# Kernel optimization log

Measured on AMD Instinct MI355X. Metric: run time of the kernel, lower is better.

## Reference

```python
import jax, jax.numpy as jnp
import numpy as np


def _quantize(x, weight):
    # x: (B, D, H, W); weight: (D, K)
    B, D, H, W = x.shape
    K = weight.shape[1]
    xf = x.reshape(B, D, H * W)  # (B, D, N)
    x2 = jnp.sum(xf * xf, axis=1)                      # (B, N)
    cross = jnp.einsum('bdn,dk->bnk', xf, weight)       # (B, N, K)
    e2 = jnp.sum(weight * weight, axis=0)               # (K,)
    d2 = x2[..., None] - 2.0 * cross + e2               # (B, N, K)
    argmin = jnp.argmin(d2, axis=-1)                    # (B, N)
    # gather codes: (B, N, D) -> (B, D, N) -> (B, D, H, W)
    quant = weight.T[argmin]                            # (B, N, D)
    result = jnp.transpose(quant, (0, 2, 1)).reshape(B, D, H, W)
    return result, argmin.reshape(B, H, W)


def setup_inputs() -> dict:
    key = jax.random.key(0)
    k1, k2 = jax.random.split(key)
    x = jax.random.normal(k1, (32, 256, 32, 32), dtype=jnp.float32)
    weight = jax.random.uniform(k2, (256, 512), dtype=jnp.float32)  # torch.rand init
    return {"x": x, "weight": weight}


def reference(x, weight):
    result, argmin = _quantize(x, weight)
    return result, argmin
```

## Files before the change

### kernel.cpp

```cpp
#include <hip/hip_runtime.h>

typedef __attribute__((ext_vector_type(8))) short bf16x8;
typedef __attribute__((ext_vector_type(16))) float f32x16;

__device__ __forceinline__ bool lex_lt(float av, int ai, float bv, int bi) {
  return av < bv || (av == bv && ai < bi);
}

__device__ __forceinline__ unsigned bf16_rne(float v) {
  unsigned u = __float_as_uint(v);
  return (u + 0x7fffu + ((u >> 16) & 1u)) >> 16;
}

__device__ __forceinline__ unsigned pk_bf16(float a, float b) {
  return bf16_rne(a) | (bf16_rne(b) << 16);
}

__global__ __launch_bounds__(256) void vq_pre(
    const float* __restrict__ w, float* __restrict__ e2,
    short* __restrict__ wtil, float* __restrict__ wT) {
  int blk = blockIdx.x;
  if (blk < 64) {
    int gid = blk * 256 + threadIdx.x;
    int n  = gid & 511;
    int kg = gid >> 9;
    bf16x8 hv, lv;
    float vv[8];
#pragma unroll
    for (int j = 0; j < 8; ++j) {
      float v = w[(kg * 8 + j) * 512 + n];
      vv[j] = v;
      unsigned h = bf16_rne(v);
      float hf = __uint_as_float(h << 16);
      unsigned l = bf16_rne(v - hf);
      hv[j] = (short)h;
      lv[j] = (short)l;
    }
    short* dst = wtil + (size_t)gid * 8;
    *(bf16x8*)dst = hv;
    *(bf16x8*)(dst + 131072) = lv;
    if (wT) {
      float* p = wT + (size_t)n * 256 + kg * 8;
      *(float4*)p       = make_float4(vv[0], vv[1], vv[2], vv[3]);
      *(float4*)(p + 4) = make_float4(vv[4], vv[5], vv[6], vv[7]);
    }
  } else {
    int t = (blk - 64) * 256 + threadIdx.x;
    int k = t >> 2;
    int part = t & 3;
    double s = 0.0;
#pragma unroll 8
    for (int d = part * 64; d < part * 64 + 64; ++d) {
      double v = (double)w[d * 512 + k];
      s = fma(v, v, s);
    }
    s += __shfl_xor(s, 1);
    s += __shfl_xor(s, 2);
    if (part == 0) e2[k] = (float)s;
  }
}

__global__ __launch_bounds__(512, 4) void vq_main(
    const float* __restrict__ x, const float* __restrict__ w,
    const float* __restrict__ e2g, const short* __restrict__ wtil,
    const float* __restrict__ wT,
    float* __restrict__ out, float* __restrict__ arg_out) {
  __shared__ __align__(16) char arena[76800];
  short* xh   = (short*)arena;
  short* xl   = (short*)(arena + 32768);
  float* e2s  = (float*)(arena + 65536);
  float* tv1  = (float*)(arena + 67584);
  float* tv2  = (float*)(arena + 69632);
  int*   ti1  = (int*)(arena + 71680);
  int*   ti2  = (int*)(arena + 73728);
  int*   p1S  = (int*)(arena + 75776);
  int*   p2S  = (int*)(arena + 76032);
  int*   needS= (int*)(arena + 76288);
  int*   rpickS=(int*)(arena + 76544);
  float* gbuf = (float*)arena;

  const int tid = threadIdx.x;
  const int b  = blockIdx.x >> 4;
  const int n0 = (blockIdx.x & 15) << 6;
  const float* xbase = x + (size_t)b * 262144 + n0;

  {
    const int n4  = tid & 15;
    const int kgp = tid >> 4;
    float4 v[8];
#pragma unroll
    for (int j = 0; j < 8; ++j)
      v[j] = *(const float4*)(xbase + (size_t)(kgp * 8 + j) * 1024 + (n4 << 2));
#pragma unroll
    for (int i = 0; i < 4; ++i) {
      int m = (n4 << 2) + i;
      union { int w4[4]; bf16x8 v8; } H, L;
#pragma unroll
      for (int jj = 0; jj < 4; ++jj) {
        float a = (i == 0) ? v[2*jj].x : (i == 1) ? v[2*jj].y : (i == 2) ? v[2*jj].z : v[2*jj].w;
        float c = (i == 0) ? v[2*jj+1].x : (i == 1) ? v[2*jj+1].y : (i == 2) ? v[2*jj+1].z : v[2*jj+1].w;
        unsigned hu = pk_bf16(a, c);
        float haf = __uint_as_float(hu << 16);
        float hcf = __uint_as_float(hu & 0xffff0000u);
        unsigned lu = pk_bf16(a - haf, c - hcf);
        H.w4[jj] = (int)hu;
        L.w4[jj] = (int)lu;
      }
      int off = (m << 8) + ((kgp ^ (m & 7)) << 3);
      *(bf16x8*)&xh[off] = H.v8;
      *(bf16x8*)&xl[off] = L.v8;
    }
    e2s[tid] = e2g[tid];
  }
  __syncthreads();

  const int lane = tid & 63;
  const int wv   = tid >> 6;
  const int ln   = lane & 31;
  const int half = lane >> 5;
  const int wb   = wv << 6;

  f32x16 acc[2][2];
#pragma unroll
  for (int ct = 0; ct < 2; ++ct)
#pragma unroll
    for (int pt = 0; pt < 2; ++pt)
#pragma unroll
      for (int r = 0; r < 16; ++r) acc[ct][pt][r] = 0.f;

  const int asw = ln & 7;
  const int abase = ln << 8;

  int bofs[2];
#pragma unroll
  for (int ct = 0; ct < 2; ++ct) bofs[ct] = (wb + (ct << 5) + ln) << 3;

  bf16x8 pch[2], pcl[2];
#pragma unroll
  for (int ct = 0; ct < 2; ++ct) {
    const short* p = wtil + (half << 12) + bofs[ct];
    pch[ct] = *(const bf16x8*)p;
    pcl[ct] = *(const bf16x8*)(p + 131072);
  }

  auto kstep = [&](int ch) {
    const int kg = (ch << 1) + half;
    const int ao = abase + ((kg ^ asw) << 3);
    bf16x8 xf[2], xg[2];
#pragma unroll
    for (int pt = 0; pt < 2; ++pt) {
      xf[pt] = *(const bf16x8*)&xh[ao + (pt << 13)];
      xg[pt] = *(const bf16x8*)&xl[ao + (pt << 13)];
    }
    bf16x8 cfh[2], cfl[2];
#pragma unroll
    for (int ct = 0; ct < 2; ++ct) { cfh[ct] = pch[ct]; cfl[ct] = pcl[ct]; }
    if (ch < 15) {
      const int kgn = ((ch + 1) << 1) + half;
#pragma unroll
      for (int ct = 0; ct < 2; ++ct) {
        const short* p = wtil + (kgn << 12) + bofs[ct];
        pch[ct] = *(const bf16x8*)p;
        pcl[ct] = *(const bf16x8*)(p + 131072);
      }
    }
#pragma unroll
    for (int ct = 0; ct < 2; ++ct)
#pragma unroll
      for (int pt = 0; pt < 2; ++pt) {
        acc[ct][pt] = __builtin_amdgcn_mfma_f32_32x32x16_bf16(cfh[ct], xf[pt], acc[ct][pt], 0, 0, 0);
        acc[ct][pt] = __builtin_amdgcn_mfma_f32_32x32x16_bf16(cfh[ct], xg[pt], acc[ct][pt], 0, 0, 0);
        acc[ct][pt] = __builtin_amdgcn_mfma_f32_32x32x16_bf16(cfl[ct], xf[pt], acc[ct][pt], 0, 0, 0);
      }
  };

  kstep(0);  kstep(1);  kstep(2);  kstep(3);
  kstep(4);  kstep(5);  kstep(6);  kstep(7);
  kstep(8);  kstep(9);  kstep(10); kstep(11);
  kstep(12); kstep(13); kstep(14); kstep(15);

  float e2r[2][16];
#pragma unroll
  for (int ct = 0; ct < 2; ++ct)
#pragma unroll
    for (int r = 0; r < 16; ++r)
      e2r[ct][r] = e2s[wb + (ct << 5) + (r & 3) + ((r >> 2) << 3) + (half << 2)];

#pragma unroll
  for (int pt = 0; pt < 2; ++pt) {
    float v1 = 3.4e38f, v2 = 3.4e38f;
    int i1 = 0x7fffffff, i2 = 0x7fffffff;
#pragma unroll
    for (int ct = 0; ct < 2; ++ct) {
#pragma unroll
      for (int r = 0; r < 16; ++r) {
        int k = wb + (ct << 5) + (r & 3) + ((r >> 2) << 3) + (half << 2);
        float s = fmaf(-2.f, acc[ct][pt][r], e2r[ct][r]);
        if (lex_lt(s, k, v1, i1)) { v2 = v1; i2 = i1; v1 = s; i1 = k; }
        else if (lex_lt(s, k, v2, i2)) { v2 = s; i2 = k; }
      }
    }
    {
      float ov1 = __shfl_xor(v1, 32);
      int   oi1 = __shfl_xor(i1, 32);
      float ov2 = __shfl_xor(v2, 32);
      int   oi2 = __shfl_xor(i2, 32);
      bool aFirst = lex_lt(v1, i1, ov1, oi1);
      float nv1 = aFirst ? v1 : ov1;  int ni1 = aFirst ? i1 : oi1;
      float cv  = aFirst ? ov1 : v1;  int ci  = aFirst ? oi1 : i1;
      float sv  = aFirst ? v2 : ov2;  int si  = aFirst ? i2 : oi2;
      bool cFirst = lex_lt(cv, ci, sv, si);
      v1 = nv1; i1 = ni1;
      v2 = cFirst ? cv : sv; i2 = cFirst ? ci : si;
    }
    if (half == 0) {
      int s = (wv << 6) + (pt << 5) + ln;
      tv1[s] = v1; ti1[s] = i1; tv2[s] = v2; ti2[s] = i2;
    }
  }
  __syncthreads();

  if (tid < 64) {
    int row = tid;
    float v1 = 3.4e38f, v2 = 3.4e38f;
    int i1 = 0x7fffffff, i2 = 0x7fffffff;
#pragma unroll
    for (int wvv = 0; wvv < 8; ++wvv) {
      int s = (wvv << 6) + row;
      float a1 = tv1[s]; int ai = ti1[s];
      float a2 = tv2[s]; int bi = ti2[s];
      if (lex_lt(a1, ai, v1, i1)) { v2 = v1; i2 = i1; v1 = a1; i1 = ai; }
      else if (lex_lt(a1, ai, v2, i2)) { v2 = a1; i2 = ai; }
      if (lex_lt(a2, bi, v1, i1)) { v2 = v1; i2 = i1; v1 = a2; i1 = bi; }
      else if (lex_lt(a2, bi, v2, i2)) { v2 = a2; i2 = bi; }
    }
    p1S[row] = i1; p2S[row] = i2;
    needS[row] = (v2 - v1 < 0.01f) ? 1 : 0;
    rpickS[row] = i1;
  }
  __syncthreads();

  for (int t = 0; t < 8; ++t) {
    int row = (t << 3) + wv;
    if (needS[row]) {
      int i1 = p1S[row], i2 = p2S[row];
      const float* xp = x + (size_t)b * 262144 + n0 + row;
      double s1 = 0.0, s2 = 0.0;
      int k0 = lane << 2;
#pragma unroll
      for (int i = 0; i < 4; ++i) {
        int k = k0 + i;
        double xv = (double)xp[(size_t)k * 1024];
        double w1 = (double)w[k * 512 + i1];
        double w2 = (double)w[k * 512 + i2];
        double t1 = xv - w1, t2 = xv - w2;
        s1 = fma(t1, t1, s1);
        s2 = fma(t2, t2, s2);
      }
#pragma unroll
      for (int off = 32; off >= 1; off >>= 1) {
        s1 += __shfl_xor(s1, off);
        s2 += __shfl_xor(s2, off);
      }
      if (lane == 0 && (s2 < s1 || (s2 == s1 && i2 < i1))) rpickS[row] = i2;
    }
  }
  __syncthreads();

  if (tid < 64) arg_out[b * 1024 + n0 + tid] = (float)rpickS[tid];

  if (wT) {
    {
      const int pos  = tid >> 3;
      const int dseg = tid & 7;
      const float* wrow = wT + (size_t)rpickS[pos] * 256;
#pragma unroll
      for (int j = 0; j < 8; ++j) {
        int d0 = (j << 5) + (dseg << 2);
        float4 v = *(const float4*)(wrow + d0);
        gbuf[(d0 + 0) * 68 + pos] = v.x;
        gbuf[(d0 + 1) * 68 + pos] = v.y;
        gbuf[(d0 + 2) * 68 + pos] = v.z;
        gbuf[(d0 + 3) * 68 + pos] = v.w;
      }
    }
    __syncthreads();
    {
      const int nn0 = (tid & 15) << 2;
      const int d0g = tid >> 4;
      float* obase = out + (size_t)b * 262144 + n0 + nn0;
#pragma unroll
      for (int dg = 0; dg < 8; ++dg) {
        int d = d0g + (dg << 5);
        float4 o = *(const float4*)&gbuf[d * 68 + nn0];
        *(float4*)(obase + (size_t)d * 1024) = o;
      }
    }
  } else {
    const int nn0 = (tid & 15) << 2;
    const int d0g = tid >> 4;
    int pk0 = rpickS[nn0], pk1 = rpickS[nn0 + 1], pk2 = rpickS[nn0 + 2], pk3 = rpickS[nn0 + 3];
    float* obase = out + (size_t)b * 262144 + n0 + nn0;
#pragma unroll
    for (int dg = 0; dg < 8; ++dg) {
      int d = d0g + (dg << 5);
      const float* wr = w + d * 512;
      float4 o = make_float4(wr[pk0], wr[pk1], wr[pk2], wr[pk3]);
      *(float4*)(obase + (size_t)d * 1024) = o;
    }
  }
}

extern "C" void kernel_launch(void* const* d_in, const int* in_sizes, int n_in,
                              void* d_out, int out_size, void* d_ws, size_t ws_size,
                              hipStream_t stream) {
  const float* x = (const float*)d_in[0];
  const float* w = (const float*)d_in[1];
  float* out  = (float*)d_out;
  float* argf = out + 8388608;
  float* e2   = (float*)d_ws;
  short* wtil = (short*)((char*)d_ws + 2048);
  size_t need = 2048 + 524288 + 524288;
  float* wT   = (ws_size >= need) ? (float*)((char*)d_ws + 2048 + 524288) : nullptr;

  vq_pre<<<72, 256, 0, stream>>>(w, e2, wtil, wT);
  vq_main<<<512, 512, 0, stream>>>(x, w, e2, wtil, wT, out, argf);
}
```

Baseline: 115.9 us.

## Fuse codebook preprocessing into main kernel with a software grid barrier

Merges the weight-splitting and codebook-norm kernel into the main VQ kernel. The first 36 blocks do the preprocessing, and all 512 blocks then meet at an atomic grid-wide barrier before the MFMA phase. The goal is to remove a kernel launch and overlap preprocessing with the x conversion into LDS. This relies on all 512 blocks being co-resident: with 4 blocks per CU of 512 threads on 256 CUs that likely holds, but if it does not, the spin-with-timeout break can let blocks read stale data. It also adds a memset launch to reset the barrier counter.

```diff
diff --git a/kernel.cpp b/kernel.cpp
--- a/kernel.cpp
+++ b/kernel.cpp
@@ -16,54 +16,23 @@
   return bf16_rne(a) | (bf16_rne(b) << 16);
 }
 
-__global__ __launch_bounds__(256) void vq_pre(
-    const float* __restrict__ w, float* __restrict__ e2,
-    short* __restrict__ wtil, float* __restrict__ wT) {
-  int blk = blockIdx.x;
-  if (blk < 64) {
-    int gid = blk * 256 + threadIdx.x;
-    int n  = gid & 511;
-    int kg = gid >> 9;
-    bf16x8 hv, lv;
-    float vv[8];
-#pragma unroll
-    for (int j = 0; j < 8; ++j) {
-      float v = w[(kg * 8 + j) * 512 + n];
-      vv[j] = v;
-      unsigned h = bf16_rne(v);
-      float hf = __uint_as_float(h << 16);
-      unsigned l = bf16_rne(v - hf);
-      hv[j] = (short)h;
-      lv[j] = (short)l;
-    }
-    short* dst = wtil + (size_t)gid * 8;
-    *(bf16x8*)dst = hv;
-    *(bf16x8*)(dst + 131072) = lv;
-    if (wT) {
-      float* p = wT + (size_t)n * 256 + kg * 8;
-      *(float4*)p       = make_float4(vv[0], vv[1], vv[2], vv[3]);
-      *(float4*)(p + 4) = make_float4(vv[4], vv[5], vv[6], vv[7]);
-    }
-  } else {
-    int t = (blk - 64) * 256 + threadIdx.x;
-    int k = t >> 2;
-    int part = t & 3;
-    double s = 0.0;
-#pragma unroll 8
-    for (int d = part * 64; d < part * 64 + 64; ++d) {
-      double v = (double)w[d * 512 + k];
-      s = fma(v, v, s);
-    }
-    s += __shfl_xor(s, 1);
-    s += __shfl_xor(s, 2);
-    if (part == 0) e2[k] = (float)s;
-  }
-}
-
-__global__ __launch_bounds__(512, 4) void vq_main(
+__device__ __forceinline__ void grid_barrier(unsigned* bar) {
+  __syncthreads();
+  if (threadIdx.x == 0) {
+    __hip_atomic_fetch_add(bar, 1u, __ATOMIC_RELEASE, __HIP_MEMORY_SCOPE_AGENT);
+    long spins = 0;
+    while (__hip_atomic_load(bar, __ATOMIC_ACQUIRE, __HIP_MEMORY_SCOPE_AGENT) < 512u) {
+      __builtin_amdgcn_s_sleep(1);
+      if (++spins > (1L << 22)) break;
+    }
+  }
+  __syncthreads();
+}
+
+__global__ __launch_bounds__(512, 4) void vq_fused(
     const float* __restrict__ x, const float* __restrict__ w,
-    const float* __restrict__ e2g, const short* __restrict__ wtil,
-    const float* __restrict__ wT,
+    float* __restrict__ e2g, short* __restrict__ wtil,
+    float* __restrict__ wT, unsigned* __restrict__ bar,
     float* __restrict__ out, float* __restrict__ arg_out) {
   __shared__ __align__(16) char arena[76800];
   short* xh   = (short*)arena;
@@ -80,8 +49,49 @@
   float* gbuf = (float*)arena;
 
   const int tid = threadIdx.x;
-  const int b  = blockIdx.x >> 4;
-  const int n0 = (blockIdx.x & 15) << 6;
+  const int bid = blockIdx.x;
+
+  if (bid < 32) {
+    int gid = bid * 512 + tid;
+    int n  = gid & 511;
+    int kg = gid >> 9;
+    bf16x8 hv, lv;
+    float vv[8];
+#pragma unroll
+    for (int j = 0; j < 8; ++j) {
+      float v = w[(kg * 8 + j) * 512 + n];
+      vv[j] = v;
+      unsigned h = bf16_rne(v);
+      float hf = __uint_as_float(h << 16);
+      unsigned l = bf16_rne(v - hf);
+      hv[j] = (short)h;
+      lv[j] = (short)l;
+    }
+    short* dst = wtil + (size_t)gid * 8;
+    *(bf16x8*)dst = hv;
+    *(bf16x8*)(dst + 131072) = lv;
+    if (wT) {
+      float* p = wT + (size_t)n * 256 + kg * 8;
+      *(float4*)p       = make_float4(vv[0], vv[1], vv[2], vv[3]);
+      *(float4*)(p + 4) = make_float4(vv[4], vv[5], vv[6], vv[7]);
+    }
+  } else if (bid < 36) {
+    int t = (bid - 32) * 512 + tid;
+    int k = t >> 2;
+    int part = t & 3;
+    double s = 0.0;
+#pragma unroll 8
+    for (int d = part * 64; d < part * 64 + 64; ++d) {
+      double v = (double)w[d * 512 + k];
+      s = fma(v, v, s);
+    }
+    s += __shfl_xor(s, 1);
+    s += __shfl_xor(s, 2);
+    if (part == 0) e2g[k] = (float)s;
+  }
+
+  const int b  = bid >> 4;
+  const int n0 = (bid & 15) << 6;
   const float* xbase = x + (size_t)b * 262144 + n0;
 
   {
@@ -110,9 +120,9 @@
       *(bf16x8*)&xh[off] = H.v8;
       *(bf16x8*)&xl[off] = L.v8;
     }
-    e2s[tid] = e2g[tid];
-  }
-  __syncthreads();
+  }
+
+  grid_barrier(bar);
 
   const int lane = tid & 63;
   const int wv   = tid >> 6;
@@ -178,6 +188,9 @@
   kstep(4);  kstep(5);  kstep(6);  kstep(7);
   kstep(8);  kstep(9);  kstep(10); kstep(11);
   kstep(12); kstep(13); kstep(14); kstep(15);
+
+  e2s[tid] = e2g[tid];
+  __syncthreads();
 
   float e2r[2][16];
 #pragma unroll
@@ -320,9 +333,10 @@
   float* argf = out + 8388608;
   float* e2   = (float*)d_ws;
   short* wtil = (short*)((char*)d_ws + 2048);
-  size_t need = 2048 + 524288 + 524288;
+  size_t need = 2048 + 524288 + 524288 + (1 << 21) + 64;
   float* wT   = (ws_size >= need) ? (float*)((char*)d_ws + 2048 + 524288) : nullptr;
-
-  vq_pre<<<72, 256, 0, stream>>>(w, e2, wtil, wT);
-  vq_main<<<512, 512, 0, stream>>>(x, w, e2, wtil, wT, out, argf);
-}
+  unsigned* bar = (unsigned*)((char*)d_ws + (1 << 21));
+
+  hipMemsetAsync(bar, 0, 64, stream);
+  vq_fused<<<512, 512, 0, stream>>>(x, w, e2, wtil, wT, bar, out, argf);
+}
```

Measured after the change: 174.7 us. +50.7%, slower.

## Halve per-block position tile to raise occupancy and drop codebook register prefetch

Applied to the files above, without the earlier changes.

Each block now handles 32 positions instead of 64, which halves LDS use and accumulator registers and doubles the grid to 1024 blocks. Launch bounds rise to 8 waves per SIMD. The software prefetch of codebook fragments is replaced by direct loads inside each k-step. Each codebook fragment is now reused by only one position tile instead of two, so global/L2 traffic for the bf16 codebook doubles and load latency is exposed unless the higher occupancy hides it.

```diff
diff --git a/kernel.cpp b/kernel.cpp
--- a/kernel.cpp
+++ b/kernel.cpp
@@ -60,45 +60,46 @@
   }
 }
 
-__global__ __launch_bounds__(512, 4) void vq_main(
+__global__ __launch_bounds__(512, 8) void vq_main(
     const float* __restrict__ x, const float* __restrict__ w,
     const float* __restrict__ e2g, const short* __restrict__ wtil,
     const float* __restrict__ wT,
     float* __restrict__ out, float* __restrict__ arg_out) {
-  __shared__ __align__(16) char arena[76800];
+  __shared__ __align__(16) char arena[39424];
   short* xh   = (short*)arena;
-  short* xl   = (short*)(arena + 32768);
-  float* e2s  = (float*)(arena + 65536);
-  float* tv1  = (float*)(arena + 67584);
-  float* tv2  = (float*)(arena + 69632);
-  int*   ti1  = (int*)(arena + 71680);
-  int*   ti2  = (int*)(arena + 73728);
-  int*   p1S  = (int*)(arena + 75776);
-  int*   p2S  = (int*)(arena + 76032);
-  int*   needS= (int*)(arena + 76288);
-  int*   rpickS=(int*)(arena + 76544);
+  short* xl   = (short*)(arena + 16384);
+  float* e2s  = (float*)(arena + 32768);
+  float* tv1  = (float*)(arena + 34816);
+  float* tv2  = (float*)(arena + 35840);
+  int*   ti1  = (int*)(arena + 36864);
+  int*   ti2  = (int*)(arena + 37888);
+  int*   p1S  = (int*)(arena + 38912);
+  int*   p2S  = (int*)(arena + 39040);
+  int*   needS= (int*)(arena + 39168);
+  int*   rpickS=(int*)(arena + 39296);
   float* gbuf = (float*)arena;
 
   const int tid = threadIdx.x;
-  const int b  = blockIdx.x >> 4;
-  const int n0 = (blockIdx.x & 15) << 6;
+  const int b  = blockIdx.x >> 5;
+  const int n0 = (blockIdx.x & 31) << 5;
   const float* xbase = x + (size_t)b * 262144 + n0;
 
   {
-    const int n4  = tid & 15;
+    e2s[tid] = e2g[tid];
+    const int n2  = tid & 15;
     const int kgp = tid >> 4;
-    float4 v[8];
+    float2 v[8];
 #pragma unroll
     for (int j = 0; j < 8; ++j)
-      v[j] = *(const float4*)(xbase + (size_t)(kgp * 8 + j) * 1024 + (n4 << 2));
-#pragma unroll
-    for (int i = 0; i < 4; ++i) {
-      int m = (n4 << 2) + i;
+      v[j] = *(const float2*)(xbase + (size_t)(kgp * 8 + j) * 1024 + (n2 << 1));
+#pragma unroll
+    for (int i = 0; i < 2; ++i) {
+      int m = (n2 << 1) + i;
       union { int w4[4]; bf16x8 v8; } H, L;
 #pragma unroll
       for (int jj = 0; jj < 4; ++jj) {
-        float a = (i == 0) ? v[2*jj].x : (i == 1) ? v[2*jj].y : (i == 2) ? v[2*jj].z : v[2*jj].w;
-        float c = (i == 0) ? v[2*jj+1].x : (i == 1) ? v[2*jj+1].y : (i == 2) ? v[2*jj+1].z : v[2*jj+1].w;
+        float a = (i == 0) ? v[2*jj].x   : v[2*jj].y;
+        float c = (i == 0) ? v[2*jj+1].x : v[2*jj+1].y;
         unsigned hu = pk_bf16(a, c);
         float haf = __uint_as_float(hu << 16);
         float hcf = __uint_as_float(hu & 0xffff0000u);
@@ -110,7 +111,6 @@
       *(bf16x8*)&xh[off] = H.v8;
       *(bf16x8*)&xl[off] = L.v8;
     }
-    e2s[tid] = e2g[tid];
   }
   __syncthreads();
 
@@ -120,13 +120,11 @@
   const int half = lane >> 5;
   const int wb   = wv << 6;
 
-  f32x16 acc[2][2];
+  f32x16 acc[2];
 #pragma unroll
   for (int ct = 0; ct < 2; ++ct)
 #pragma unroll
-    for (int pt = 0; pt < 2; ++pt)
-#pragma unroll
-      for (int r = 0; r < 16; ++r) acc[ct][pt][r] = 0.f;
+    for (int r = 0; r < 16; ++r) acc[ct][r] = 0.f;
 
   const int asw = ln & 7;
   const int abase = ln << 8;
@@ -134,44 +132,24 @@
   int bofs[2];
 #pragma unroll
   for (int ct = 0; ct < 2; ++ct) bofs[ct] = (wb + (ct << 5) + ln) << 3;
-
-  bf16x8 pch[2], pcl[2];
-#pragma unroll
-  for (int ct = 0; ct < 2; ++ct) {
-    const short* p = wtil + (half << 12) + bofs[ct];
-    pch[ct] = *(const bf16x8*)p;
-    pcl[ct] = *(const bf16x8*)(p + 131072);
-  }
 
   auto kstep = [&](int ch) {
     const int kg = (ch << 1) + half;
     const int ao = abase + ((kg ^ asw) << 3);
-    bf16x8 xf[2], xg[2];
-#pragma unroll
-    for (int pt = 0; pt < 2; ++pt) {
-      xf[pt] = *(const bf16x8*)&xh[ao + (pt << 13)];
-      xg[pt] = *(const bf16x8*)&xl[ao + (pt << 13)];
-    }
-    bf16x8 cfh[2], cfl[2];
-#pragma unroll
-    for (int ct = 0; ct < 2; ++ct) { cfh[ct] = pch[ct]; cfl[ct] = pcl[ct]; }
-    if (ch < 15) {
-      const int kgn = ((ch + 1) << 1) + half;
-#pragma unroll
-      for (int ct = 0; ct < 2; ++ct) {
-        const short* p = wtil + (kgn << 12) + bofs[ct];
-        pch[ct] = *(const bf16x8*)p;
-        pcl[ct] = *(const bf16x8*)(p + 131072);
-      }
-    }
-#pragma unroll
-    for (int ct = 0; ct < 2; ++ct)
-#pragma unroll
-      for (int pt = 0; pt < 2; ++pt) {
-        acc[ct][pt] = __builtin_amdgcn_mfma_f32_32x32x16_bf16(cfh[ct], xf[pt], acc[ct][pt], 0, 0, 0);
-        acc[ct][pt] = __builtin_amdgcn_mfma_f32_32x32x16_bf16(cfh[ct], xg[pt], acc[ct][pt], 0, 0, 0);
-        acc[ct][pt] = __builtin_amdgcn_mfma_f32_32x32x16_bf16(cfl[ct], xf[pt], acc[ct][pt], 0, 0, 0);
-      }
+    bf16x8 xf = *(const bf16x8*)&xh[ao];
+    bf16x8 xg = *(const bf16x8*)&xl[ao];
+    const short* p0 = wtil + (kg << 12) + bofs[0];
+    const short* p1 = wtil + (kg << 12) + bofs[1];
+    bf16x8 ch0 = *(const bf16x8*)p0;
+    bf16x8 cl0 = *(const bf16x8*)(p0 + 131072);
+    bf16x8 ch1 = *(const bf16x8*)p1;
+    bf16x8 cl1 = *(const bf16x8*)(p1 + 131072);
+    acc[0] = __builtin_amdgcn_mfma_f32_32x32x16_bf16(ch0, xf, acc[0], 0, 0, 0);
+    acc[0] = __builtin_amdgcn_mfma_f32_32x32x16_bf16(ch0, xg, acc[0], 0, 0, 0);
+    acc[0] = __builtin_amdgcn_mfma_f32_32x32x16_bf16(cl0, xf, acc[0], 0, 0, 0);
+    acc[1] = __builtin_amdgcn_mfma_f32_32x32x16_bf16(ch1, xf, acc[1], 0, 0, 0);
+    acc[1] = __builtin_amdgcn_mfma_f32_32x32x16_bf16(ch1, xg, acc[1], 0, 0, 0);
+    acc[1] = __builtin_amdgcn_mfma_f32_32x32x16_bf16(cl1, xf, acc[1], 0, 0, 0);
   };
 
   kstep(0);  kstep(1);  kstep(2);  kstep(3);
@@ -179,15 +157,7 @@
   kstep(8);  kstep(9);  kstep(10); kstep(11);
   kstep(12); kstep(13); kstep(14); kstep(15);
 
-  float e2r[2][16];
-#pragma unroll
-  for (int ct = 0; ct < 2; ++ct)
-#pragma unroll
-    for (int r = 0; r < 16; ++r)
-      e2r[ct][r] = e2s[wb + (ct << 5) + (r & 3) + ((r >> 2) << 3) + (half << 2)];
-
-#pragma unroll
-  for (int pt = 0; pt < 2; ++pt) {
+  {
     float v1 = 3.4e38f, v2 = 3.4e38f;
     int i1 = 0x7fffffff, i2 = 0x7fffffff;
 #pragma unroll
@@ -195,7 +165,7 @@
 #pragma unroll
       for (int r = 0; r < 16; ++r) {
         int k = wb + (ct << 5) + (r & 3) + ((r >> 2) << 3) + (half << 2);
-        float s = fmaf(-2.f, acc[ct][pt][r], e2r[ct][r]);
+        float s = fmaf(-2.f, acc[ct][r], e2s[k]);
         if (lex_lt(s, k, v1, i1)) { v2 = v1; i2 = i1; v1 = s; i1 = k; }
         else if (lex_lt(s, k, v2, i2)) { v2 = s; i2 = k; }
       }
@@ -214,19 +184,19 @@
       v2 = cFirst ? cv : sv; i2 = cFirst ? ci : si;
     }
     if (half == 0) {
-      int s = (wv << 6) + (pt << 5) + ln;
+      int s = (wv << 5) + ln;
       tv1[s] = v1; ti1[s] = i1; tv2[s] = v2; ti2[s] = i2;
     }
   }
   __syncthreads();
 
-  if (tid < 64) {
+  if (tid < 32) {
     int row = tid;
     float v1 = 3.4e38f, v2 = 3.4e38f;
     int i1 = 0x7fffffff, i2 = 0x7fffffff;
 #pragma unroll
     for (int wvv = 0; wvv < 8; ++wvv) {
-      int s = (wvv << 6) + row;
+      int s = (wvv << 5) + row;
       float a1 = tv1[s]; int ai = ti1[s];
       float a2 = tv2[s]; int bi = ti2[s];
       if (lex_lt(a1, ai, v1, i1)) { v2 = v1; i2 = i1; v1 = a1; i1 = ai; }
@@ -240,7 +210,7 @@
   }
   __syncthreads();
 
-  for (int t = 0; t < 8; ++t) {
+  for (int t = 0; t < 4; ++t) {
     int row = (t << 3) + wv;
     if (needS[row]) {
       int i1 = p1S[row], i2 = p2S[row];
@@ -267,43 +237,43 @@
   }
   __syncthreads();
 
-  if (tid < 64) arg_out[b * 1024 + n0 + tid] = (float)rpickS[tid];
+  if (tid < 32) arg_out[b * 1024 + n0 + tid] = (float)rpickS[tid];
 
   if (wT) {
     {
-      const int pos  = tid >> 3;
-      const int dseg = tid & 7;
+      const int pos  = tid >> 4;
+      const int dseg = tid & 15;
       const float* wrow = wT + (size_t)rpickS[pos] * 256;
 #pragma unroll
-      for (int j = 0; j < 8; ++j) {
-        int d0 = (j << 5) + (dseg << 2);
+      for (int j = 0; j < 4; ++j) {
+        int d0 = (j << 6) + (dseg << 2);
         float4 v = *(const float4*)(wrow + d0);
-        gbuf[(d0 + 0) * 68 + pos] = v.x;
-        gbuf[(d0 + 1) * 68 + pos] = v.y;
-        gbuf[(d0 + 2) * 68 + pos] = v.z;
-        gbuf[(d0 + 3) * 68 + pos] = v.w;
+        gbuf[(d0 + 0) * 36 + pos] = v.x;
+        gbuf[(d0 + 1) * 36 + pos] = v.y;
+        gbuf[(d0 + 2) * 36 + pos] = v.z;
+        gbuf[(d0 + 3) * 36 + pos] = v.w;
       }
     }
     __syncthreads();
     {
-      const int nn0 = (tid & 15) << 2;
-      const int d0g = tid >> 4;
+      const int nn0 = (tid & 7) << 2;
+      const int d0g = tid >> 3;
       float* obase = out + (size_t)b * 262144 + n0 + nn0;
 #pragma unroll
-      for (int dg = 0; dg < 8; ++dg) {
-        int d = d0g + (dg << 5);
-        float4 o = *(const float4*)&gbuf[d * 68 + nn0];
+      for (int dg = 0; dg < 4; ++dg) {
+        int d = d0g + (dg << 6);
+        float4 o = *(const float4*)&gbuf[d * 36 + nn0];
         *(float4*)(obase + (size_t)d * 1024) = o;
       }
     }
   } else {
-    const int nn0 = (tid & 15) << 2;
-    const int d0g = tid >> 4;
+    const int nn0 = (tid & 7) << 2;
+    const int d0g = tid >> 3;
     int pk0 = rpickS[nn0], pk1 = rpickS[nn0 + 1], pk2 = rpickS[nn0 + 2], pk3 = rpickS[nn0 + 3];
     float* obase = out + (size_t)b * 262144 + n0 + nn0;
 #pragma unroll
-    for (int dg = 0; dg < 8; ++dg) {
-      int d = d0g + (dg << 5);
+    for (int dg = 0; dg < 4; ++dg) {
+      int d = d0g + (dg << 6);
       const float* wr = w + d * 512;
       float4 o = make_float4(wr[pk0], wr[pk1], wr[pk2], wr[pk3]);
       *(float4*)(obase + (size_t)d * 1024) = o;
@@ -324,5 +294,5 @@
   float* wT   = (ws_size >= need) ? (float*)((char*)d_ws + 2048 + 524288) : nullptr;
 
   vq_pre<<<72, 256, 0, stream>>>(w, e2, wtil, wT);
-  vq_main<<<512, 512, 0, stream>>>(x, w, e2, wtil, wT, out, argf);
-}
+  vq_main<<<1024, 512, 0, stream>>>(x, w, e2, wtil, wT, out, argf);
+}
```

Measured after the change: 121.2 us. 1.05x slower.

## Strengthen LDS swizzle, stagger per-wave K start, and prefetch x fragments

Applied to the files above, without the earlier changes.

Adds a second XOR term (row>>3) to the LDS swizzle for the bf16 hi/lo x tiles, intended to remove remaining bank conflicts on the MFMA operand reads. Each wave now starts its K loop at a different chunk offset and wraps around, spreading simultaneous global reads of the codebook across different addresses. The x fragments are also double-buffered in registers alongside the codebook prefetch. Register pressure rises, the loop carries a leftover unused index computation, and accumulation order now differs per wave, which could shift argmin results on near-ties.

```diff
diff --git a/kernel.cpp b/kernel.cpp
--- a/kernel.cpp
+++ b/kernel.cpp
@@ -85,6 +85,7 @@
   const float* xbase = x + (size_t)b * 262144 + n0;
 
   {
+    e2s[tid] = e2g[tid];
     const int n4  = tid & 15;
     const int kgp = tid >> 4;
     float4 v[8];
@@ -106,11 +107,11 @@
         H.w4[jj] = (int)hu;
         L.w4[jj] = (int)lu;
       }
-      int off = (m << 8) + ((kgp ^ (m & 7)) << 3);
+      int slot = kgp ^ (m & 7) ^ ((m >> 3) & 7);
+      int off = (m << 8) + (slot << 3);
       *(bf16x8*)&xh[off] = H.v8;
       *(bf16x8*)&xl[off] = L.v8;
     }
-    e2s[tid] = e2g[tid];
   }
   __syncthreads();
 
@@ -128,56 +129,61 @@
 #pragma unroll
       for (int r = 0; r < 16; ++r) acc[ct][pt][r] = 0.f;
 
-  const int asw = ln & 7;
+  const int sw    = (ln & 7) ^ (ln >> 3);
   const int abase = ln << 8;
 
   int bofs[2];
 #pragma unroll
   for (int ct = 0; ct < 2; ++ct) bofs[ct] = (wb + (ct << 5) + ln) << 3;
 
-  bf16x8 pch[2], pcl[2];
-#pragma unroll
-  for (int ct = 0; ct < 2; ++ct) {
-    const short* p = wtil + (half << 12) + bofs[ct];
-    pch[ct] = *(const bf16x8*)p;
-    pcl[ct] = *(const bf16x8*)(p + 131072);
-  }
-
-  auto kstep = [&](int ch) {
-    const int kg = (ch << 1) + half;
-    const int ao = abase + ((kg ^ asw) << 3);
-    bf16x8 xf[2], xg[2];
-#pragma unroll
-    for (int pt = 0; pt < 2; ++pt) {
-      xf[pt] = *(const bf16x8*)&xh[ao + (pt << 13)];
-      xg[pt] = *(const bf16x8*)&xl[ao + (pt << 13)];
-    }
-    bf16x8 cfh[2], cfl[2];
-#pragma unroll
-    for (int ct = 0; ct < 2; ++ct) { cfh[ct] = pch[ct]; cfl[ct] = pcl[ct]; }
-    if (ch < 15) {
-      const int kgn = ((ch + 1) << 1) + half;
-#pragma unroll
-      for (int ct = 0; ct < 2; ++ct) {
-        const short* p = wtil + (kgn << 12) + bofs[ct];
-        pch[ct] = *(const bf16x8*)p;
-        pcl[ct] = *(const bf16x8*)(p + 131072);
-      }
+  const int st = (wv & 7) << 1;
+
+  bf16x8 xf[2], xg[2], pch[2], pcl[2];
+  {
+    const int kg = (st << 1) + half;
+    const int s0 = ((kg ^ sw) << 3);
+    const int a0 = abase + s0;
+    const int a1 = abase + 8192 + (s0 ^ 32);
+    xf[0] = *(const bf16x8*)&xh[a0]; xg[0] = *(const bf16x8*)&xl[a0];
+    xf[1] = *(const bf16x8*)&xh[a1]; xg[1] = *(const bf16x8*)&xl[a1];
+    const short* p0 = wtil + (kg << 12) + bofs[0];
+    const short* p1 = wtil + (kg << 12) + bofs[1];
+    pch[0] = *(const bf16x8*)p0; pcl[0] = *(const bf16x8*)(p0 + 131072);
+    pch[1] = *(const bf16x8*)p1; pcl[1] = *(const bf16x8*)(p1 + 131072);
+  }
+
+#pragma unroll
+  for (int i = 0; i < 16; ++i) {
+    bf16x8 cxf[2], cxg[2], cch[2], ccl[2];
+#pragma unroll
+    for (int q = 0; q < 2; ++q) {
+      cxf[q] = xf[q]; cxg[q] = xg[q]; cch[q] = pch[q]; ccl[q] = pcl[q];
+    }
+    if (i < 15) {
+      const int kgn = ((((st >> 1) + i + 1) & 15) << 2) + (half << 1)
+                      - (((st >> 1) + i + 1) & 15) * 2;
+      const int cn  = (st + i + 1) & 15;
+      const int kg2 = (cn << 1) + half;
+      const int s0  = ((kg2 ^ sw) << 3);
+      const int a0  = abase + s0;
+      const int a1  = abase + 8192 + (s0 ^ 32);
+      xf[0] = *(const bf16x8*)&xh[a0]; xg[0] = *(const bf16x8*)&xl[a0];
+      xf[1] = *(const bf16x8*)&xh[a1]; xg[1] = *(const bf16x8*)&xl[a1];
+      const short* p0 = wtil + (kg2 << 12) + bofs[0];
+      const short* p1 = wtil + (kg2 << 12) + bofs[1];
+      pch[0] = *(const bf16x8*)p0; pcl[0] = *(const bf16x8*)(p0 + 131072);
+      pch[1] = *(const bf16x8*)p1; pcl[1] = *(const bf16x8*)(p1 + 131072);
+      (void)kgn;
     }
 #pragma unroll
     for (int ct = 0; ct < 2; ++ct)
 #pragma unroll
       for (int pt = 0; pt < 2; ++pt) {
-        acc[ct][pt] = __builtin_amdgcn_mfma_f32_32x32x16_bf16(cfh[ct], xf[pt], acc[ct][pt], 0, 0, 0);
-        acc[ct][pt] = __builtin_amdgcn_mfma_f32_32x32x16_bf16(cfh[ct], xg[pt], acc[ct][pt], 0, 0, 0);
-        acc[ct][pt] = __builtin_amdgcn_mfma_f32_32x32x16_bf16(cfl[ct], xf[pt], acc[ct][pt], 0, 0, 0);
-      }
-  };
-
-  kstep(0);  kstep(1);  kstep(2);  kstep(3);
-  kstep(4);  kstep(5);  kstep(6);  kstep(7);
-  kstep(8);  kstep(9);  kstep(10); kstep(11);
-  kstep(12); kstep(13); kstep(14); kstep(15);
+        acc[ct][pt] = __builtin_amdgcn_mfma_f32_32x32x16_bf16(cch[ct], cxf[pt], acc[ct][pt], 0, 0, 0);
+        acc[ct][pt] = __builtin_amdgcn_mfma_f32_32x32x16_bf16(cch[ct], cxg[pt], acc[ct][pt], 0, 0, 0);
+        acc[ct][pt] = __builtin_amdgcn_mfma_f32_32x32x16_bf16(ccl[ct], cxf[pt], acc[ct][pt], 0, 0, 0);
+      }
+  }
 
   float e2r[2][16];
 #pragma unroll
```

After: 117.0 us. No clear change (+0.9%).
